# Kernel optimization log

Measured on AMD Instinct MI355X. Metric: run time of the kernel, lower is better.

Reference implementation:

```python
import jax, jax.numpy as jnp
import numpy as np

# HRR ops (holoformer): bind = circular convolution via FFT; unbind = circular
# correlation (bind with the approximate inverse), i.e. conj in freq domain.

def _fft(a):
    return jnp.fft.fft(a, axis=-1)

def _bind_f(Fa, Fb):
    return jnp.fft.ifft(Fa * Fb, axis=-1).real

def _unbind_f(Fs, Fk):
    return jnp.fft.ifft(Fs * jnp.conj(Fk), axis=-1).real


def setup_inputs() -> dict:
    key = jax.random.key(0)
    B, S, D = 4, 4096, 1024
    ks = jax.random.split(key, 5)
    scale = 1.0 / np.sqrt(D)
    inp = {
        "x": jax.random.normal(ks[0], (B, S, D), dtype=jnp.float32),
        "Wq": jax.random.normal(ks[1], (D, D), dtype=jnp.float32) * scale,
        "bq": jnp.zeros((D,), jnp.float32),
        "Wk": jax.random.normal(ks[2], (D, D), dtype=jnp.float32) * scale,
        "bk": jnp.zeros((D,), jnp.float32),
        "Wv": jax.random.normal(ks[3], (D, D), dtype=jnp.float32) * scale,
        "bv": jnp.zeros((D,), jnp.float32),
        "Wr": jax.random.normal(ks[4], (D, D), dtype=jnp.float32) * scale,
        "br": jnp.zeros((D,), jnp.float32),
    }
    return inp


def reference(x, Wq, bq, Wk, bk, Wv, bv, Wr, br):
    # tanh-gated linear projections (nn.Linear stores weight as [out, in])
    query = jnp.tanh(jnp.einsum('bsd,ed->bse', x, Wq) + bq)
    keys = jnp.tanh(jnp.einsum('bsd,ed->bse', x, Wk) + bk)
    values = jnp.tanh(jnp.einsum('bsd,ed->bse', x, Wv) + bv)
    remove_query = jnp.tanh(jnp.einsum('bsd,ed->bse', x, Wr) + br)

    # bind(keys, values) and sum over sequence -> s: (B, 1, D)
    x_k = _bind_f(_fft(keys), _fft(values))
    s = x_k.sum(axis=1, keepdims=True)
    Fs = _fft(s)

    # retrieve with query, add
    retrieved = _unbind_f(Fs, _fft(query))
    out = x + retrieved

    # remove: bind(remove_query, unbind(s, remove_query))
    Fr = _fft(remove_query)
    remove_values = _unbind_f(Fs, Fr)
    removes = _bind_f(Fr, _fft(remove_values))
    out = out - removes
    return out
```

## Files before the change

### kernel.cpp

```cpp
#include <hip/hip_runtime.h>
#include <hip/hip_fp16.h>

#define D 1024
#define LOG2D 10
#define S_LEN 4096
#define BATCH 4
#define NROWS (BATCH * S_LEN)
#define PI_F 3.14159265358979323846f

#define SLOT(p) ((p) + ((p) >> 4))
#define FBUF 1088
#define NTW 341

typedef _Float16 f16x8 __attribute__((ext_vector_type(8)));
typedef float f32x4 __attribute__((ext_vector_type(4)));

__device__ __forceinline__ float2 cmul(float2 a, float2 b) {
    return make_float2(a.x * b.x - a.y * b.y, a.x * b.y + a.y * b.x);
}

__device__ __forceinline__ float fast_tanh(float v) {
    float e = __expf(2.0f * v);
    return 1.0f - 2.0f * __builtin_amdgcn_rcpf(e + 1.0f);
}

__device__ __forceinline__ void g2lds16(const void* g, void* l) {
    __builtin_amdgcn_global_load_lds(
        (const __attribute__((address_space(1))) unsigned int*)g,
        (__attribute__((address_space(3))) unsigned int*)l, 16, 0, 0);
}

__global__ __launch_bounds__(256) void convert_all(
    const float* __restrict__ x,
    const float* __restrict__ w0, const float* __restrict__ w1,
    const float* __restrict__ w2, const float* __restrict__ w3,
    __half* __restrict__ xh,
    __half* __restrict__ h0, __half* __restrict__ h1,
    __half* __restrict__ h2, __half* __restrict__ h3)
{
    const int b = blockIdx.x;
    const float* s;
    __half* d;
    int li;
    if (b < 16384) { s = x; d = xh; li = b; }
    else {
        int t = b - 16384;
        int r = t >> 10;
        li = t & 1023;
        s = (r == 0) ? w0 : (r == 1) ? w1 : (r == 2) ? w2 : w3;
        d = (r == 0) ? h0 : (r == 1) ? h1 : (r == 2) ? h2 : h3;
    }
    const int idx = li * 256 + threadIdx.x;
    float4 v = ((const float4*)s)[idx];
    __half2 lo = __floats2half2_rn(v.x, v.y);
    __half2 hi = __floats2half2_rn(v.z, v.w);
    ((__half2*)d)[2 * idx + 0] = lo;
    ((__half2*)d)[2 * idx + 1] = hi;
}

__global__ __launch_bounds__(256, 2) void gemm_mfma2(
    const __half* __restrict__ Xh,
    const __half* __restrict__ W0, const float* __restrict__ b0, __half* __restrict__ O0,
    const __half* __restrict__ W1, const float* __restrict__ b1, __half* __restrict__ O1)
{
    const int idx = blockIdx.x;
    const int xcd = idx & 7;
    const int j = idx >> 3;
    const int n0 = (j & 7) * 128;
    const int m0 = (xcd * 16 + (j >> 3)) * 128;

    __shared__ __align__(16) __half As[128 * 32];
    __shared__ __align__(16) __half B0s[128 * 32];
    __shared__ __align__(16) __half B1s[128 * 32];

    const int tid = threadIdx.x;
    const int wave = tid >> 6;
    const int lane = tid & 63;

    const int srow = lane >> 2;
    const int schunk = (lane & 3) ^ ((lane >> 3) & 3);

    const __half* gA[2];
    const __half* gB0[2];
    const __half* gB1[2];
    __half* lA[2];
    __half* lB0[2];
    __half* lB1[2];
#pragma unroll
    for (int c = 0; c < 2; ++c) {
        const int rg = (wave * 2 + c) * 16 + srow;
        gA[c]  = Xh + (size_t)(m0 + rg) * 1024 + schunk * 8;
        gB0[c] = W0 + (size_t)(n0 + rg) * 1024 + schunk * 8;
        gB1[c] = W1 + (size_t)(n0 + rg) * 1024 + schunk * 8;
        lA[c]  = As  + (wave * 2 + c) * 512;
        lB0[c] = B0s + (wave * 2 + c) * 512;
        lB1[c] = B1s + (wave * 2 + c) * 512;
    }

    const int wm = (wave & 1) * 64;
    const int wn = (wave >> 1) * 64;
    const int quad = lane >> 4;
    const int l15 = lane & 15;

    int aoff[4], boff[4];
#pragma unroll
    for (int i = 0; i < 4; ++i) {
        const int Ra = wm + i * 16 + l15;
        aoff[i] = Ra * 32 + (quad ^ ((Ra >> 1) & 3)) * 8;
        const int Rb = wn + i * 16 + l15;
        boff[i] = Rb * 32 + (quad ^ ((Rb >> 1) & 3)) * 8;
    }

    f32x4 acc0[4][4], acc1[4][4];
#pragma unroll
    for (int i = 0; i < 4; ++i)
#pragma unroll
        for (int jj = 0; jj < 4; ++jj) {
            acc0[i][jj] = (f32x4){0.f, 0.f, 0.f, 0.f};
            acc1[i][jj] = (f32x4){0.f, 0.f, 0.f, 0.f};
        }

    for (int kt = 0; kt < 32; ++kt) {
        const int kh = kt * 32;
        __syncthreads();
        g2lds16(gA[0] + kh, lA[0]);
        g2lds16(gA[1] + kh, lA[1]);
        g2lds16(gB0[0] + kh, lB0[0]);
        g2lds16(gB0[1] + kh, lB0[1]);
        g2lds16(gB1[0] + kh, lB1[0]);
        g2lds16(gB1[1] + kh, lB1[1]);
        __syncthreads();

        f16x8 af[4], bf0[4], bf1[4];
#pragma unroll
        for (int i = 0; i < 4; ++i) af[i] = *(const f16x8*)(As + aoff[i]);
#pragma unroll
        for (int jj = 0; jj < 4; ++jj) {
            bf0[jj] = *(const f16x8*)(B0s + boff[jj]);
            bf1[jj] = *(const f16x8*)(B1s + boff[jj]);
        }
#pragma unroll
        for (int i = 0; i < 4; ++i)
#pragma unroll
            for (int jj = 0; jj < 4; ++jj) {
                acc0[i][jj] = __builtin_amdgcn_mfma_f32_16x16x32_f16(af[i], bf0[jj], acc0[i][jj], 0, 0, 0);
                acc1[i][jj] = __builtin_amdgcn_mfma_f32_16x16x32_f16(af[i], bf1[jj], acc1[i][jj], 0, 0, 0);
            }
    }

#pragma unroll
    for (int jj = 0; jj < 4; ++jj) {
        const int n = n0 + wn + jj * 16 + l15;
        const float bv0 = b0[n];
        const float bv1 = b1[n];
#pragma unroll
        for (int i = 0; i < 4; ++i) {
            const int mbase = m0 + wm + i * 16 + quad * 4;
#pragma unroll
            for (int r = 0; r < 4; ++r) {
                O0[(size_t)(mbase + r) * 1024 + n] = __float2half(fast_tanh(acc0[i][jj][r] + bv0));
                O1[(size_t)(mbase + r) * 1024 + n] = __float2half(fast_tanh(acc1[i][jj][r] + bv1));
            }
        }
    }
}

__device__ __forceinline__ void build_twiddles_r4(float2* Wts, int tid) {
    for (int j = tid; j < NTW; j += 256) {
        int k, m;
        if (j == 0)      { k = 0;      m = 1;   }
        else if (j < 5)  { k = j - 1;  m = 4;   }
        else if (j < 21) { k = j - 5;  m = 16;  }
        else if (j < 85) { k = j - 21; m = 64;  }
        else             { k = j - 85; m = 256; }
        float ang = PI_F * (float)k / (2.0f * (float)m);
        Wts[j] = make_float2(cosf(ang), -sinf(ang));
    }
}

__device__ void fft1024_r4(float2* bufA, float2* bufB, const float2* Wts,
                           float dir, int tid) {
    float2* src = bufA;
    float2* dst = bufB;
    int m = 1;
#pragma unroll
    for (int s = 0; s < 5; ++s) {
        __syncthreads();
        const int k = tid & (m - 1);
        const int jb = tid >> (2 * s);
        float2 x0 = src[SLOT(tid)];
        float2 x1 = src[SLOT(tid + 256)];
        float2 x2 = src[SLOT(tid + 512)];
        float2 x3 = src[SLOT(tid + 768)];
        float2 y1, y2, y3;
        if (s == 0) { y1 = x1; y2 = x2; y3 = x3; }
        else {
            const int soff = (m - 1) / 3;
            float2 t1 = Wts[soff + k];
            t1.y *= dir;
            float2 t2 = cmul(t1, t1);
            float2 t3 = cmul(t1, t2);
            y1 = cmul(x1, t1);
            y2 = cmul(x2, t2);
            y3 = cmul(x3, t3);
        }
        float2 a = make_float2(x0.x + y2.x, x0.y + y2.y);
        float2 b = make_float2(x0.x - y2.x, x0.y - y2.y);
        float2 c = make_float2(y1.x + y3.x, y1.y + y3.y);
        float2 d = make_float2(y1.x - y3.x, y1.y - y3.y);
        float2 e = make_float2(dir * d.y, -dir * d.x);
        const int o = (jb << (2 * s + 2)) + k;
        dst[SLOT(o)]         = make_float2(a.x + c.x, a.y + c.y);
        dst[SLOT(o + m)]     = make_float2(b.x + e.x, b.y + e.y);
        dst[SLOT(o + 2 * m)] = make_float2(a.x - c.x, a.y - c.y);
        dst[SLOT(o + 3 * m)] = make_float2(b.x - e.x, b.y - e.y);
        float2* t = src; src = dst; dst = t;
        m <<= 2;
    }
    __syncthreads();
}

#define ROWS_PER_BLOCK 8
__global__ __launch_bounds__(256) void bind_accum_kernel(
    const __half* __restrict__ K, const __half* __restrict__ V, float2* __restrict__ Fs)
{
    __shared__ __align__(16) float2 bufA[FBUF];
    __shared__ __align__(16) float2 bufB[FBUF];
    __shared__ __align__(16) float2 Wts[NTW];
    const int tid = threadIdx.x;
    build_twiddles_r4(Wts, tid);

    const int row0 = blockIdx.x * ROWS_PER_BLOCK;
    const int b = row0 >> 12;

    float2 accr[4];
#pragma unroll
    for (int h = 0; h < 4; ++h) accr[h] = make_float2(0.f, 0.f);

    for (int r = 0; r < ROWS_PER_BLOCK; ++r) {
        const size_t base = (size_t)(row0 + r) * D;
#pragma unroll
        for (int h = 0; h < 4; ++h) {
            const int j = tid + (h << 8);
            bufA[SLOT(j)] = make_float2(__half2float(K[base + j]), __half2float(V[base + j]));
        }
        fft1024_r4(bufA, bufB, Wts, 1.0f, tid);
#pragma unroll
        for (int h = 0; h < 4; ++h) {
            const int j = tid + (h << 8);
            const int j2 = (D - j) & (D - 1);
            float2 Zt = bufB[SLOT(j)];
            float2 Zc = bufB[SLOT(j2)]; Zc.y = -Zc.y;
            float2 Fk = make_float2(0.5f * (Zt.x + Zc.x), 0.5f * (Zt.y + Zc.y));
            float2 Fv = make_float2(0.5f * (Zt.y - Zc.y), -0.5f * (Zt.x - Zc.x));
            float2 P = cmul(Fk, Fv);
            accr[h].x += P.x; accr[h].y += P.y;
        }
    }
#pragma unroll
    for (int h = 0; h < 4; ++h) {
        const int j = tid + (h << 8);
        atomicAdd(&Fs[(size_t)b * D + j].x, accr[h].x);
        atomicAdd(&Fs[(size_t)b * D + j].y, accr[h].y);
    }
}

__global__ __launch_bounds__(256) void retrieve_kernel(
    const __half* __restrict__ Q, const __half* __restrict__ R,
    const float2* __restrict__ Fs, const float* __restrict__ x, float* __restrict__ out)
{
    __shared__ __align__(16) float2 bufA[FBUF];
    __shared__ __align__(16) float2 bufB[FBUF];
    __shared__ __align__(16) float2 Wts[NTW];
    const int tid = threadIdx.x;
    build_twiddles_r4(Wts, tid);

    const int row = blockIdx.x;
    const int b = row >> 12;
    const size_t base = (size_t)row * D;

#pragma unroll
    for (int h = 0; h < 4; ++h) {
        const int j = tid + (h << 8);
        bufA[SLOT(j)] = make_float2(__half2float(Q[base + j]), __half2float(R[base + j]));
    }
    fft1024_r4(bufA, bufB, Wts, 1.0f, tid);

#pragma unroll
    for (int h = 0; h < 4; ++h) {
        const int j = tid + (h << 8);
        const int j2 = (D - j) & (D - 1);
        float2 Zt = bufB[SLOT(j)];
        float2 Zc = bufB[SLOT(j2)]; Zc.y = -Zc.y;
        float2 Fq = make_float2(0.5f * (Zt.x + Zc.x), 0.5f * (Zt.y + Zc.y));
        float2 Fr = make_float2(0.5f * (Zt.y - Zc.y), -0.5f * (Zt.x - Zc.x));
        float2 g  = make_float2(Fq.x - (Fr.x * Fr.x + Fr.y * Fr.y), -Fq.y);
        float2 Ff = Fs[(size_t)b * D + j];
        bufA[SLOT(j)] = cmul(Ff, g);
    }
    fft1024_r4(bufA, bufB, Wts, -1.0f, tid);

    const float inv = 1.0f / (float)D;
#pragma unroll
    for (int h = 0; h < 4; ++h) {
        const int j = tid + (h << 8);
        out[base + j] = x[base + j] + bufB[SLOT(j)].x * inv;
    }
}

extern "C" void kernel_launch(void* const* d_in, const int* in_sizes, int n_in,
                              void* d_out, int out_size, void* d_ws, size_t ws_size,
                              hipStream_t stream) {
    const float* x  = (const float*)d_in[0];
    const float* Wq = (const float*)d_in[1];
    const float* bq = (const float*)d_in[2];
    const float* Wk = (const float*)d_in[3];
    const float* bk = (const float*)d_in[4];
    const float* Wv = (const float*)d_in[5];
    const float* bv = (const float*)d_in[6];
    const float* Wr = (const float*)d_in[7];
    const float* br = (const float*)d_in[8];
    float* out = (float*)d_out;

    __half* P0 = (__half*)d_ws;
    __half* P1 = (__half*)((char*)d_ws + (size_t)NROWS * D * 2);
    float2* Fs = (float2*)((char*)d_ws + (size_t)NROWS * D * 4);

    __half* Xh  = (__half*)d_out;
    __half* Whk = (__half*)d_out + (size_t)16 * 1024 * 1024;
    __half* Whv = Whk + (size_t)1024 * 1024;
    __half* Whq = Whv + (size_t)1024 * 1024;
    __half* Whr = Whq + (size_t)1024 * 1024;

    convert_all<<<16384 + 4 * 1024, 256, 0, stream>>>(
        x, Wk, Wv, Wq, Wr, Xh, Whk, Whv, Whq, Whr);

    hipMemsetAsync(Fs, 0, (size_t)BATCH * D * sizeof(float2), stream);

    gemm_mfma2<<<1024, 256, 0, stream>>>(Xh, Whk, bk, P0, Whv, bv, P1);
    bind_accum_kernel<<<NROWS / ROWS_PER_BLOCK, 256, 0, stream>>>(P0, P1, Fs);
    gemm_mfma2<<<1024, 256, 0, stream>>>(Xh, Whq, bq, P0, Whr, br, P1);
    retrieve_kernel<<<NROWS, 256, 0, stream>>>(P0, P1, Fs, x, out);
}
```

Before: 472.3 us.

## Run each 1024-point FFT on a single 64-lane wavefront with vectorized fp16 loads

The bind and retrieve kernels drop from 256 threads to 64, so each row's FFT is handled by one wavefront. Each lane now processes four radix-4 butterflies per stage and sixteen output bins. The fp16 K/V and Q/R rows are loaded as 8-wide vectors per lane instead of scalar halves. This is meant to cheapen the __syncthreads barriers and raise the number of resident blocks, at the cost of more serial work and registers per thread. It also keeps the same LDS footprint per block, which may now cap occupancy instead.

```diff
diff --git a/kernel.cpp b/kernel.cpp
--- a/kernel.cpp
+++ b/kernel.cpp
@@ -166,7 +166,7 @@
 }
 
 __device__ __forceinline__ void build_twiddles_r4(float2* Wts, int tid) {
-    for (int j = tid; j < NTW; j += 256) {
+    for (int j = tid; j < NTW; j += 64) {
         int k, m;
         if (j == 0)      { k = 0;      m = 1;   }
         else if (j < 5)  { k = j - 1;  m = 4;   }
@@ -178,42 +178,46 @@
     }
 }
 
-__device__ void fft1024_r4(float2* bufA, float2* bufB, const float2* Wts,
-                           float dir, int tid) {
+__device__ void fft1024_r4_w64(float2* bufA, float2* bufB, const float2* Wts,
+                               float dir, int lane) {
     float2* src = bufA;
     float2* dst = bufB;
     int m = 1;
 #pragma unroll
     for (int s = 0; s < 5; ++s) {
         __syncthreads();
-        const int k = tid & (m - 1);
-        const int jb = tid >> (2 * s);
-        float2 x0 = src[SLOT(tid)];
-        float2 x1 = src[SLOT(tid + 256)];
-        float2 x2 = src[SLOT(tid + 512)];
-        float2 x3 = src[SLOT(tid + 768)];
-        float2 y1, y2, y3;
-        if (s == 0) { y1 = x1; y2 = x2; y3 = x3; }
-        else {
-            const int soff = (m - 1) / 3;
-            float2 t1 = Wts[soff + k];
-            t1.y *= dir;
-            float2 t2 = cmul(t1, t1);
-            float2 t3 = cmul(t1, t2);
-            y1 = cmul(x1, t1);
-            y2 = cmul(x2, t2);
-            y3 = cmul(x3, t3);
-        }
-        float2 a = make_float2(x0.x + y2.x, x0.y + y2.y);
-        float2 b = make_float2(x0.x - y2.x, x0.y - y2.y);
-        float2 c = make_float2(y1.x + y3.x, y1.y + y3.y);
-        float2 d = make_float2(y1.x - y3.x, y1.y - y3.y);
-        float2 e = make_float2(dir * d.y, -dir * d.x);
-        const int o = (jb << (2 * s + 2)) + k;
-        dst[SLOT(o)]         = make_float2(a.x + c.x, a.y + c.y);
-        dst[SLOT(o + m)]     = make_float2(b.x + e.x, b.y + e.y);
-        dst[SLOT(o + 2 * m)] = make_float2(a.x - c.x, a.y - c.y);
-        dst[SLOT(o + 3 * m)] = make_float2(b.x - e.x, b.y - e.y);
+#pragma unroll
+        for (int u = 0; u < 4; ++u) {
+            const int i = lane + (u << 6);
+            const int k = i & (m - 1);
+            const int jb = i >> (2 * s);
+            float2 x0 = src[SLOT(i)];
+            float2 x1 = src[SLOT(i + 256)];
+            float2 x2 = src[SLOT(i + 512)];
+            float2 x3 = src[SLOT(i + 768)];
+            float2 y1, y2, y3;
+            if (s == 0) { y1 = x1; y2 = x2; y3 = x3; }
+            else {
+                const int soff = (m - 1) / 3;
+                float2 t1 = Wts[soff + k];
+                t1.y *= dir;
+                float2 t2 = cmul(t1, t1);
+                float2 t3 = cmul(t1, t2);
+                y1 = cmul(x1, t1);
+                y2 = cmul(x2, t2);
+                y3 = cmul(x3, t3);
+            }
+            float2 a = make_float2(x0.x + y2.x, x0.y + y2.y);
+            float2 b = make_float2(x0.x - y2.x, x0.y - y2.y);
+            float2 c = make_float2(y1.x + y3.x, y1.y + y3.y);
+            float2 d = make_float2(y1.x - y3.x, y1.y - y3.y);
+            float2 e = make_float2(dir * d.y, -dir * d.x);
+            const int o = (jb << (2 * s + 2)) + k;
+            dst[SLOT(o)]         = make_float2(a.x + c.x, a.y + c.y);
+            dst[SLOT(o + m)]     = make_float2(b.x + e.x, b.y + e.y);
+            dst[SLOT(o + 2 * m)] = make_float2(a.x - c.x, a.y - c.y);
+            dst[SLOT(o + 3 * m)] = make_float2(b.x - e.x, b.y - e.y);
+        }
         float2* t = src; src = dst; dst = t;
         m <<= 2;
     }
@@ -221,33 +225,38 @@
 }
 
 #define ROWS_PER_BLOCK 8
-__global__ __launch_bounds__(256) void bind_accum_kernel(
+__global__ __launch_bounds__(64) void bind_accum_kernel(
     const __half* __restrict__ K, const __half* __restrict__ V, float2* __restrict__ Fs)
 {
     __shared__ __align__(16) float2 bufA[FBUF];
     __shared__ __align__(16) float2 bufB[FBUF];
     __shared__ __align__(16) float2 Wts[NTW];
-    const int tid = threadIdx.x;
-    build_twiddles_r4(Wts, tid);
+    const int lane = threadIdx.x;
+    build_twiddles_r4(Wts, lane);
 
     const int row0 = blockIdx.x * ROWS_PER_BLOCK;
     const int b = row0 >> 12;
 
-    float2 accr[4];
-#pragma unroll
-    for (int h = 0; h < 4; ++h) accr[h] = make_float2(0.f, 0.f);
+    float2 accr[16];
+#pragma unroll
+    for (int h = 0; h < 16; ++h) accr[h] = make_float2(0.f, 0.f);
 
     for (int r = 0; r < ROWS_PER_BLOCK; ++r) {
         const size_t base = (size_t)(row0 + r) * D;
-#pragma unroll
-        for (int h = 0; h < 4; ++h) {
-            const int j = tid + (h << 8);
-            bufA[SLOT(j)] = make_float2(__half2float(K[base + j]), __half2float(V[base + j]));
-        }
-        fft1024_r4(bufA, bufB, Wts, 1.0f, tid);
-#pragma unroll
-        for (int h = 0; h < 4; ++h) {
-            const int j = tid + (h << 8);
+        const f16x8* Kv = (const f16x8*)(K + base);
+        const f16x8* Vv = (const f16x8*)(V + base);
+        f16x8 k0 = Kv[lane * 2], k1 = Kv[lane * 2 + 1];
+        f16x8 v0 = Vv[lane * 2], v1 = Vv[lane * 2 + 1];
+        __syncthreads();
+#pragma unroll
+        for (int t = 0; t < 8; ++t) {
+            bufA[SLOT(lane * 16 + t)]     = make_float2((float)k0[t], (float)v0[t]);
+            bufA[SLOT(lane * 16 + 8 + t)] = make_float2((float)k1[t], (float)v1[t]);
+        }
+        fft1024_r4_w64(bufA, bufB, Wts, 1.0f, lane);
+#pragma unroll
+        for (int h = 0; h < 16; ++h) {
+            const int j = lane + (h << 6);
             const int j2 = (D - j) & (D - 1);
             float2 Zt = bufB[SLOT(j)];
             float2 Zc = bufB[SLOT(j2)]; Zc.y = -Zc.y;
@@ -258,37 +267,41 @@
         }
     }
 #pragma unroll
-    for (int h = 0; h < 4; ++h) {
-        const int j = tid + (h << 8);
+    for (int h = 0; h < 16; ++h) {
+        const int j = lane + (h << 6);
         atomicAdd(&Fs[(size_t)b * D + j].x, accr[h].x);
         atomicAdd(&Fs[(size_t)b * D + j].y, accr[h].y);
     }
 }
 
-__global__ __launch_bounds__(256) void retrieve_kernel(
+__global__ __launch_bounds__(64) void retrieve_kernel(
     const __half* __restrict__ Q, const __half* __restrict__ R,
     const float2* __restrict__ Fs, const float* __restrict__ x, float* __restrict__ out)
 {
     __shared__ __align__(16) float2 bufA[FBUF];
     __shared__ __align__(16) float2 bufB[FBUF];
     __shared__ __align__(16) float2 Wts[NTW];
-    const int tid = threadIdx.x;
-    build_twiddles_r4(Wts, tid);
+    const int lane = threadIdx.x;
+    build_twiddles_r4(Wts, lane);
 
     const int row = blockIdx.x;
     const int b = row >> 12;
     const size_t base = (size_t)row * D;
 
-#pragma unroll
-    for (int h = 0; h < 4; ++h) {
-        const int j = tid + (h << 8);
-        bufA[SLOT(j)] = make_float2(__half2float(Q[base + j]), __half2float(R[base + j]));
-    }
-    fft1024_r4(bufA, bufB, Wts, 1.0f, tid);
-
-#pragma unroll
-    for (int h = 0; h < 4; ++h) {
-        const int j = tid + (h << 8);
+    const f16x8* Qv = (const f16x8*)(Q + base);
+    const f16x8* Rv = (const f16x8*)(R + base);
+    f16x8 q0 = Qv[lane * 2], q1 = Qv[lane * 2 + 1];
+    f16x8 r0 = Rv[lane * 2], r1 = Rv[lane * 2 + 1];
+#pragma unroll
+    for (int t = 0; t < 8; ++t) {
+        bufA[SLOT(lane * 16 + t)]     = make_float2((float)q0[t], (float)r0[t]);
+        bufA[SLOT(lane * 16 + 8 + t)] = make_float2((float)q1[t], (float)r1[t]);
+    }
+    fft1024_r4_w64(bufA, bufB, Wts, 1.0f, lane);
+
+#pragma unroll
+    for (int h = 0; h < 16; ++h) {
+        const int j = lane + (h << 6);
         const int j2 = (D - j) & (D - 1);
         float2 Zt = bufB[SLOT(j)];
         float2 Zc = bufB[SLOT(j2)]; Zc.y = -Zc.y;
@@ -298,12 +311,12 @@
         float2 Ff = Fs[(size_t)b * D + j];
         bufA[SLOT(j)] = cmul(Ff, g);
     }
-    fft1024_r4(bufA, bufB, Wts, -1.0f, tid);
+    fft1024_r4_w64(bufA, bufB, Wts, -1.0f, lane);
 
     const float inv = 1.0f / (float)D;
 #pragma unroll
-    for (int h = 0; h < 4; ++h) {
-        const int j = tid + (h << 8);
+    for (int h = 0; h < 16; ++h) {
+        const int j = lane + (h << 6);
         out[base + j] = x[base + j] + bufB[SLOT(j)].x * inv;
     }
 }
@@ -338,7 +351,7 @@
     hipMemsetAsync(Fs, 0, (size_t)BATCH * D * sizeof(float2), stream);
 
     gemm_mfma2<<<1024, 256, 0, stream>>>(Xh, Whk, bk, P0, Whv, bv, P1);
-    bind_accum_kernel<<<NROWS / ROWS_PER_BLOCK, 256, 0, stream>>>(P0, P1, Fs);
+    bind_accum_kernel<<<NROWS / ROWS_PER_BLOCK, 64, 0, stream>>>(P0, P1, Fs);
     gemm_mfma2<<<1024, 256, 0, stream>>>(Xh, Whq, bq, P0, Whr, br, P1);
-    retrieve_kernel<<<NROWS, 256, 0, stream>>>(P0, P1, Fs, x, out);
-}
+    retrieve_kernel<<<NROWS, 64, 0, stream>>>(P0, P1, Fs, x, out);
+}
```

After: 537.3 us. 1.14x slower.
